# Performance work log

Hardware: AMD Instinct MI355X
Metric: run time of the kernel (lower is better)

Reference implementation:

```python
import jax, jax.numpy as jnp
import numpy as np

E = 64      # routed experts
K = 2       # top-k
CAP = 1024


def setup_inputs() -> dict:
    key = jax.random.key(0)
    ks = jax.random.split(key, 5)
    S, B, D, DFF = 2048, 4, 1024, 1408
    x = jax.random.normal(ks[0], (S, B, D), jnp.float32)
    Wg = jax.random.normal(ks[1], (D, E), jnp.float32) * 0.02
    W1 = jax.random.normal(ks[2], (E, D, DFF), jnp.float32) * 0.02
    W3 = jax.random.normal(ks[3], (E, D, DFF), jnp.float32) * 0.02
    W2 = jax.random.normal(ks[4], (E, DFF, D), jnp.float32) * 0.02
    return {"x": x, "Wg": Wg, "W1": W1, "W3": W3, "W2": W2}


def _moe(x, Wg, W1, W3, W2):
    S, B, D = x.shape
    tokens = jnp.transpose(x, (1, 0, 2)).reshape(-1, D)       # [T, D], T = B*S
    T = tokens.shape[0]

    # --- gate: softmax -> top-k, renormalize, aux loss (GShard-style) ---
    logits = tokens @ Wg                                       # [T, E]
    probs = jax.nn.softmax(logits, axis=-1)
    topk_w, topk_idx = jax.lax.top_k(probs, K)                 # [T, K]
    topk_w = topk_w / jnp.sum(topk_w, axis=-1, keepdims=True)
    me = jnp.mean(probs, axis=0)                               # [E] mean prob
    ce = jnp.mean(jax.nn.one_hot(topk_idx, E, dtype=jnp.float32).sum(1), axis=0) / K
    l_aux = E * jnp.sum(me * ce)

    # --- dispatch: per-pair slot within its expert via cumsum of one-hots ---
    flat_e = topk_idx.reshape(-1)                              # [T*K]
    oh = jax.nn.one_hot(flat_e, E, dtype=jnp.int32)            # [T*K, E]
    pos = jnp.cumsum(oh, axis=0) - 1                           # slot per expert
    slot = jnp.take_along_axis(pos, flat_e[:, None], axis=1)[:, 0]  # [T*K]
    keep = slot < CAP
    slot = jnp.where(keep, slot, 0)
    xr = jnp.repeat(tokens, K, axis=0)                         # [T*K, D]
    xr = jnp.where(keep[:, None], xr, 0.0)
    buf = jnp.zeros((E, CAP, D), x.dtype).at[flat_e, slot].add(xr)  # [E, C, D]

    # --- grouped expert FFN: SiLU-gated MLP per expert ---
    h = jax.nn.silu(jnp.einsum('ecd,edf->ecf', buf, W1)) * jnp.einsum('ecd,edf->ecf', buf, W3)
    eo = jnp.einsum('ecf,efd->ecd', h, W2)                     # [E, C, D]

    # --- combine: gather back, weight by gate probs, sum over k ---
    gathered = eo[flat_e, slot] * keep[:, None].astype(x.dtype)  # [T*K, D]
    combined = jnp.sum(gathered.reshape(T, K, D) * topk_w[..., None], axis=1)
    y = jnp.transpose(combined.reshape(B, S, D), (1, 0, 2))    # back to [S, B, D]
    return y, l_aux


def reference(x, Wg, W1, W3, W2):
    return _moe(x, Wg, W1, W3, W2)
```

## Files before the change

### kernel.cpp

```cpp
#include <hip/hip_runtime.h>
#include <hip/hip_bf16.h>


#define S_ 2048
#define B_ 4
#define D_ 1024
#define DFF_ 1408
#define E_ 64
#define T_ 8192
#define KTOP_ 2
#define NPAIR_ (T_*KTOP_)
#define PAD_ 384
#define ROWS_ (E_*PAD_)

#define BM 128
#define BN 128
#define BK 32

typedef __attribute__((ext_vector_type(8))) short short8;
typedef __attribute__((ext_vector_type(4))) short s16x4;
typedef __attribute__((ext_vector_type(4))) float f32x4;
typedef __attribute__((ext_vector_type(4))) unsigned short us4;

constexpr size_t OFF_PROBS  = 0;
constexpr size_t OFF_COUNTS = OFF_PROBS + (size_t)T_*E_*4;
constexpr size_t OFF_MESUM  = OFF_COUNTS + 512;
constexpr size_t OFF_ROWTOK = OFF_MESUM + 256;
constexpr size_t OFF_ROWW   = OFF_ROWTOK + (size_t)ROWS_*4;
constexpr size_t OFF_XBUF   = OFF_ROWW + (size_t)ROWS_*4;
constexpr size_t OFF_H      = OFF_XBUF + (size_t)ROWS_*D_*2;

__device__ __forceinline__ short f2bfs(float f) {
  union { __hip_bfloat16 h; short s; } u;
  u.h = __float2bfloat16(f);
  return u.s;
}

__device__ __forceinline__ int SWZ(int g) { return g ^ (((g >> 4) & 3) << 1); }

#define BARS() do {                                  \
    __builtin_amdgcn_sched_barrier(0);               \
    __builtin_amdgcn_s_barrier();                    \
    __builtin_amdgcn_sched_barrier(0);               \
  } while (0)
#define BARX() __builtin_amdgcn_s_barrier()
#define WAIT_LGKM0() asm volatile("s_waitcnt lgkmcnt(0)" ::: "memory")

__device__ __forceinline__ float softmax64(float acc, int lane) {
  float m = acc;
  for (int o = 32; o; o >>= 1) m = fmaxf(m, __shfl_xor(m, o));
  float p = expf(acc - m);
  float s = p;
  for (int o = 32; o; o >>= 1) s += __shfl_xor(s, o);
  return p / s;
}

__global__ __launch_bounds__(256) void gate_kernel(
    const float* __restrict__ x, const float* __restrict__ Wg,
    float* __restrict__ probs, int* __restrict__ counts,
    int* __restrict__ rowtok, float* __restrict__ roww,
    unsigned short* __restrict__ xbufO) {
  int t0 = blockIdx.x * 8;
  int tid = threadIdx.x;
  int lane = tid & 63, wv = tid >> 6;
  __shared__ float tk[8][D_];
  __shared__ int sE[8][2];
  __shared__ int sM[8][2];
  for (int u = tid; u < 8 * (D_ / 4); u += 256) {
    int r = u >> 8, c4 = u & 255;
    int t = t0 + r;
    int b = t >> 11, s = t & (S_ - 1);
    ((float4*)tk[r])[c4] = ((const float4*)(x + (size_t)(s * B_ + b) * D_))[c4];
  }
  __syncthreads();
  const float* tkA = tk[2 * wv];
  const float* tkB = tk[2 * wv + 1];
  float acc0 = 0.f, acc1 = 0.f;
  #pragma unroll 8
  for (int d = 0; d < D_; ++d) {
    float w = Wg[(size_t)d * E_ + lane];
    acc0 += tkA[d] * w;
    acc1 += tkB[d] * w;
  }
  #pragma unroll
  for (int half = 0; half < 2; ++half) {
    float p = softmax64(half ? acc1 : acc0, lane);
    int tkn = 2 * wv + half;
    int t = t0 + tkn;
    probs[(size_t)t * E_ + lane] = p;
    float v1 = p; int i1 = lane;
    for (int o = 32; o; o >>= 1) {
      float ov = __shfl_xor(v1, o); int oi = __shfl_xor(i1, o);
      if (ov > v1 || (ov == v1 && oi < i1)) { v1 = ov; i1 = oi; }
    }
    float v2 = (lane == i1) ? -1.f : p; int i2 = lane;
    for (int o = 32; o; o >>= 1) {
      float ov = __shfl_xor(v2, o); int oi = __shfl_xor(i2, o);
      if (ov > v2 || (ov == v2 && oi < i2)) { v2 = ov; i2 = oi; }
    }
    if (lane == 0) {
      float wsum = v1 + v2;
      int s1 = atomicAdd(&counts[i1], 1);
      int s2 = atomicAdd(&counts[i2], 1);
      int m1 = (s1 < PAD_) ? s1 : -1;
      int m2 = (s2 < PAD_) ? s2 : -1;
      if (m1 >= 0) { rowtok[i1 * PAD_ + m1] = t; roww[i1 * PAD_ + m1] = v1 / wsum; }
      if (m2 >= 0) { rowtok[i2 * PAD_ + m2] = t; roww[i2 * PAD_ + m2] = v2 / wsum; }
      sE[tkn][0] = i1; sM[tkn][0] = m1;
      sE[tkn][1] = i2; sM[tkn][1] = m2;
    }
  }
  __syncthreads();
  int hh = tid >> 7, t7 = tid & 127;
  #pragma unroll
  for (int pp = 0; pp < 8; ++pp) {
    int pr = 2 * pp + hh;
    int tkn = pr >> 1, j = pr & 1;
    int e = sE[tkn][j];
    int m = sM[tkn][j];
    if (m >= 0) {
      const float* src = tk[tkn] + t7 * 8;
      short8 g;
      #pragma unroll
      for (int k = 0; k < 8; ++k) g[k] = f2bfs(src[k]);
      *(short8*)(xbufO + (size_t)e * D_ * PAD_ + ((size_t)t7 * PAD_ + m) * 8) = g;
    }
  }
}

__global__ __launch_bounds__(256) void me_kernel(const float* __restrict__ probs,
                                                 float* __restrict__ mesum) {
  int e = blockIdx.x, tid = threadIdx.x;
  float a = 0.f;
  for (int t = tid; t < T_; t += 256) a += probs[(size_t)t * E_ + e];
  __shared__ float red[256];
  red[tid] = a; __syncthreads();
  for (int s = 128; s; s >>= 1) {
    if (tid < s) red[tid] += red[tid + s];
    __syncthreads();
  }
  if (tid == 0) mesum[e] = red[0];
}

__global__ __launch_bounds__(64) void finalize_kernel(
    const int* __restrict__ counts, const float* __restrict__ mesum,
    float* __restrict__ laux_out) {
  int lane = threadIdx.x;
  float contrib = (mesum[lane] / (float)T_) * ((float)counts[lane] / (float)(T_ * KTOP_));
  for (int o = 32; o; o >>= 1) contrib += __shfl_xor(contrib, o);
  if (lane == 0) laux_out[0] = (float)E_ * contrib;
}

__global__ __launch_bounds__(256, 2) void ffn1_kernel(
    const unsigned short* __restrict__ xbufO, const float* __restrict__ W1,
    const float* __restrict__ W3, const int* __restrict__ counts,
    unsigned short* __restrict__ hO) {
  int bid = blockIdx.x;
  int r = bid & 7, u = bid >> 3;
  int mb = u % 3; int v = u / 3;
  int ni = v % 11; int eg = v / 11;
  int e = eg * 8 + r;
  int n0 = ni * BN;
  int m0 = mb * BM;
  int Me = min(counts[e], PAD_);
  if (m0 >= Me) return;

  const unsigned short* AO = xbufO + (size_t)e * D_ * PAD_;
  const float* B1p = W1 + (size_t)e * D_ * DFF_ + n0;
  const float* B3p = W3 + (size_t)e * D_ * DFF_ + n0;
  unsigned short* hE = hO + (size_t)e * PAD_ * DFF_;

  __shared__ short B1s[2 * BK * BN];
  __shared__ short B3s[2 * BK * BN];
  __shared__ short Hb[BM * BN];

  int tid = threadIdx.x;
  int lane = tid & 63;
  int wv = tid >> 6, wr = wv >> 1, wc = wv & 1;

  int msel = tid >> 7;
  int t7 = tid & 127;
  int col4 = t7 & 31;
  int krow0 = (t7 >> 5) << 3;
  const float* qB = (msel ? B3p : B1p) + (size_t)krow0 * DFF_ + col4 * 4;
  char* Bdst = (char*)(msel ? B3s : B1s);
  int kseg = krow0 >> 3;
  int boffc[4];
  #pragma unroll
  for (int cc = 0; cc < 4; ++cc) {
    int c = col4 * 4 + cc;
    boffc[cc] = ((c >> 4) << 10) + (SWZ((kseg << 4) + (c & 15)) << 4);
  }

  const unsigned short* qa =
      AO + (((size_t)(lane >> 4)) * PAD_ + m0 + (wr << 6) + (lane & 15)) * 8;

  short8 afE[4], afO[4];
  f32x4 fBE[8], fBO[8];
  f32x4 acc1[4][4] = {};
  f32x4 acc3[4][4] = {};

#define F1_ALOAD(SET) do {                                               \
    _Pragma("unroll")                                                    \
    for (int mi = 0; mi < 4; ++mi)                                       \
      af##SET[mi] = *(const short8*)(qa + mi * 128);                     \
    qa += (size_t)4 * PAD_ * 8;                                          \
  } while (0)

#define F1_BLOAD(SET) do {                                               \
    _Pragma("unroll")                                                    \
    for (int j = 0; j < 8; ++j)                                          \
      fB##SET[j] = *(const f32x4*)(qB + (size_t)j * DFF_);               \
    qB += (size_t)BK * DFF_;                                             \
  } while (0)

#define F1_BWRITE(SET, BUF) do {                                         \
    _Pragma("unroll")                                                    \
    for (int cc = 0; cc < 4; ++cc) {                                     \
      short8 w;                                                          \
      _Pragma("unroll")                                                  \
      for (int j = 0; j < 8; ++j) w[j] = f2bfs(fB##SET[j][cc]);          \
      *(short8*)(Bdst + (BUF)*8192 + boffc[cc]) = w;                     \
    }                                                                    \
  } while (0)

#define F1_MFMA(BUF, SET) do {                                           \
    int lsw = SWZ(lane) << 4;                                            \
    __builtin_amdgcn_s_setprio(1);                                       \
    _Pragma("unroll")                                                    \
    for (int q = 0; q < 4; ++q) {                                        \
      short8 bf1 = *(const short8*)((char*)B1s + (BUF)*8192 + (((wc << 2) + q) << 10) + lsw); \
      short8 bf3 = *(const short8*)((char*)B3s + (BUF)*8192 + (((wc << 2) + q) << 10) + lsw); \
      _Pragma("unroll")                                                  \
      for (int mi = 0; mi < 4; ++mi) {                                   \
        acc1[mi][q] = __builtin_amdgcn_mfma_f32_16x16x32_bf16(af##SET[mi], bf1, acc1[mi][q], 0, 0, 0); \
        acc3[mi][q] = __builtin_amdgcn_mfma_f32_16x16x32_bf16(af##SET[mi], bf3, acc3[mi][q], 0, 0, 0); \
      }                                                                  \
    }                                                                    \
    __builtin_amdgcn_s_setprio(0);                                       \
  } while (0)

  F1_ALOAD(E); F1_BLOAD(E);
  F1_ALOAD(O); F1_BLOAD(O);
  for (int it = 0; it < 15; ++it) {
    F1_BWRITE(E, 0); WAIT_LGKM0(); BARS();
    F1_BLOAD(E);
    F1_MFMA(0, E);
    F1_ALOAD(E);
    BARX();
    F1_BWRITE(O, 1); WAIT_LGKM0(); BARS();
    F1_BLOAD(O);
    F1_MFMA(1, O);
    F1_ALOAD(O);
    BARX();
  }
  F1_BWRITE(E, 0); WAIT_LGKM0(); BARS(); F1_MFMA(0, E); BARX();
  F1_BWRITE(O, 1); WAIT_LGKM0(); BARS(); F1_MFMA(1, O);

  __syncthreads();
  int lr = (lane >> 4) << 2, lc = lane & 15;
  #pragma unroll
  for (int mi = 0; mi < 4; ++mi) {
    #pragma unroll
    for (int j = 0; j < 4; ++j) {
      int m = ((wr << 2) + mi) * 16 + lr + j;
      #pragma unroll
      for (int q = 0; q < 4; ++q) {
        int c = (wc << 6) + (q << 4) + lc;
        float a = acc1[mi][q][j];
        float gt = a / (1.f + __expf(-a));
        Hb[((size_t)(c >> 3) * BM + m) * 8 + (c & 7)] = f2bfs(gt * acc3[mi][q][j]);
      }
    }
  }
  __syncthreads();
  int co = tid >> 4, ml0 = (tid & 15) << 3;
  size_t fo = (size_t)(n0 >> 3) + co;
  #pragma unroll
  for (int i = 0; i < 8; ++i) {
    int ml = ml0 + i;
    short8 vq = *(const short8*)(Hb + ((size_t)co * BM + ml) * 8);
    *(short8*)(hE + (fo * PAD_ + m0 + ml) * 8) = vq;
  }
}

__global__ __launch_bounds__(256, 3) void ffn2_kernel(
    const unsigned short* __restrict__ hO, const float* __restrict__ W2,
    const int* __restrict__ counts, const int* __restrict__ rowtok,
    const float* __restrict__ roww, float* __restrict__ y) {
  int bid = blockIdx.x;
  int r = bid & 7, u = bid >> 3;
  int mb = u % 3; int v = u / 3;
  int ni = v % 8; int eg = v / 8;
  int e = eg * 8 + r;
  int n0 = ni * BN;
  int m0 = mb * BM;
  int Me = min(counts[e], PAD_);
  if (m0 >= Me) return;

  const unsigned short* AO = hO + (size_t)e * PAD_ * DFF_;
  const float* Bw = W2 + (size_t)e * DFF_ * D_ + n0;

  __shared__ short Bs[2 * BK * BN];

  int tid = threadIdx.x;
  int lane = tid & 63;
  int wv = tid >> 6, wr = wv >> 1, wc = wv & 1;

  int col4 = tid & 31;
  int krow0 = (tid >> 5) << 2;
  const float* qB = Bw + (size_t)krow0 * D_ + col4 * 4;
  int kseg = krow0 >> 3, khalf8 = ((krow0 >> 2) & 1) << 3;
  int boffc[4];
  #pragma unroll
  for (int cc = 0; cc < 4; ++cc) {
    int c = col4 * 4 + cc;
    boffc[cc] = ((c >> 4) << 10) + (SWZ((kseg << 4) + (c & 15)) << 4) + khalf8;
  }

  const unsigned short* qa =
      AO + (((size_t)(lane >> 4)) * PAD_ + m0 + (wr << 6) + (lane & 15)) * 8;

  short8 afE[4], afO[4];
  f32x4 fBE[4], fBO[4];
  f32x4 acc[4][4] = {};

#define F2_ALOAD(SET) do {                                               \
    _Pragma("unroll")                                                    \
    for (int mi = 0; mi < 4; ++mi)                                       \
      af##SET[mi] = *(const short8*)(qa + mi * 128);                     \
    qa += (size_t)4 * PAD_ * 8;                                          \
  } while (0)

#define F2_BLOAD(SET) do {                                               \
    _Pragma("unroll")                                                    \
    for (int j = 0; j < 4; ++j)                                          \
      fB##SET[j] = *(const f32x4*)(qB + (size_t)j * D_);                 \
    qB += (size_t)BK * D_;                                               \
  } while (0)

#define F2_BWRITE(SET, BUF) do {                                         \
    _Pragma("unroll")                                                    \
    for (int cc = 0; cc < 4; ++cc) {                                     \
      s16x4 w;                                                           \
      _Pragma("unroll")                                                  \
      for (int j = 0; j < 4; ++j) w[j] = f2bfs(fB##SET[j][cc]);          \
      *(s16x4*)((char*)Bs + (BUF)*8192 + boffc[cc]) = w;                 \
    }                                                                    \
  } while (0)

#define F2_MFMA(BUF, SET) do {                                           \
    int lsw = SWZ(lane) << 4;                                            \
    __builtin_amdgcn_s_setprio(1);                                       \
    _Pragma("unroll")                                                    \
    for (int q = 0; q < 4; ++q) {                                        \
      short8 bfr = *(const short8*)((char*)Bs + (BUF)*8192 + (((wc << 2) + q) << 10) + lsw); \
      _Pragma("unroll")                                                  \
      for (int mi = 0; mi < 4; ++mi)                                     \
        acc[mi][q] = __builtin_amdgcn_mfma_f32_16x16x32_bf16(af##SET[mi], bfr, acc[mi][q], 0, 0, 0); \
    }                                                                    \
    __builtin_amdgcn_s_setprio(0);                                       \
  } while (0)

  F2_ALOAD(E); F2_BLOAD(E);
  F2_ALOAD(O); F2_BLOAD(O);
  for (int it = 0; it < 21; ++it) {
    F2_BWRITE(E, 0); WAIT_LGKM0(); BARS();
    F2_BLOAD(E);
    F2_MFMA(0, E);
    F2_ALOAD(E);
    BARX();
    F2_BWRITE(O, 1); WAIT_LGKM0(); BARS();
    F2_BLOAD(O);
    F2_MFMA(1, O);
    F2_ALOAD(O);
    BARX();
  }
  F2_BWRITE(E, 0); WAIT_LGKM0(); BARS(); F2_MFMA(0, E); BARX();
  F2_BWRITE(O, 1); WAIT_LGKM0(); BARS(); F2_MFMA(1, O);

  int lr = (lane >> 4) << 2, lc = lane & 15;
  #pragma unroll
  for (int mi = 0; mi < 4; ++mi) {
    #pragma unroll
    for (int j = 0; j < 4; ++j) {
      int m = m0 + ((wr << 2) + mi) * 16 + lr + j;
      if (m < Me) {
        int rw = e * PAD_ + m;
        int t = rowtok[rw];
        float w = roww[rw];
        int b = t >> 11, s = t & (S_ - 1);
        float* yp = y + (size_t)(s * B_ + b) * D_ + n0 + (wc << 6) + lc;
        #pragma unroll
        for (int q = 0; q < 4; ++q)
          atomicAdd(&yp[q << 4], w * acc[mi][q][j]);
      }
    }
  }
}

extern "C" void kernel_launch(void* const* d_in, const int* in_sizes, int n_in,
                              void* d_out, int out_size, void* d_ws, size_t ws_size,
                              hipStream_t stream) {
  const float* x  = (const float*)d_in[0];
  const float* Wg = (const float*)d_in[1];
  const float* W1 = (const float*)d_in[2];
  const float* W3 = (const float*)d_in[3];
  const float* W2 = (const float*)d_in[4];
  float* y = (float*)d_out;
  float* laux = y + (size_t)S_ * B_ * D_;

  char* ws = (char*)d_ws;
  float* probs  = (float*)(ws + OFF_PROBS);
  int*   counts = (int*)  (ws + OFF_COUNTS);
  float* mesum  = (float*)(ws + OFF_MESUM);
  int*   rowtok = (int*)  (ws + OFF_ROWTOK);
  float* roww   = (float*)(ws + OFF_ROWW);
  unsigned short* xbufO = (unsigned short*)(ws + OFF_XBUF);
  unsigned short* hO    = (unsigned short*)(ws + OFF_H);

  hipMemsetAsync(d_out, 0, (size_t)out_size * sizeof(float), stream);
  hipMemsetAsync(counts, 0, 512, stream);

  gate_kernel<<<T_ / 8, 256, 0, stream>>>(x, Wg, probs, counts, rowtok, roww, xbufO);
  me_kernel<<<E_, 256, 0, stream>>>(probs, mesum);
  finalize_kernel<<<1, 64, 0, stream>>>(counts, mesum, laux);
  ffn1_kernel<<<8 * 8 * 11 * 3, 256, 0, stream>>>(xbufO, W1, W3, counts, hO);
  ffn2_kernel<<<8 * 8 * 8 * 3, 256, 0, stream>>>(hO, W2, counts, rowtok, roww, y);
}
```

Before: 579.9 us.

## Replace atomic scatter in FFN2 epilogue with bf16 store plus gather combine kernel

The FFN2 epilogue no longer atomically adds weighted fp32 results into the output. It now writes per-expert outputs as bf16 into the reused dispatch buffer. A new combine kernel reads each token's two expert rows using per-pair (expert, slot, weight) records from the gate, and writes y once with vector stores. This removes the output memset and the float atomics. The cost is an extra kernel launch, an extra round trip through the intermediate buffer, and bf16 rounding of expert outputs before the weighted sum.

```diff
diff --git a/kernel.cpp b/kernel.cpp
--- a/kernel.cpp
+++ b/kernel.cpp
@@ -25,15 +25,20 @@
 constexpr size_t OFF_PROBS  = 0;
 constexpr size_t OFF_COUNTS = OFF_PROBS + (size_t)T_*E_*4;
 constexpr size_t OFF_MESUM  = OFF_COUNTS + 512;
-constexpr size_t OFF_ROWTOK = OFF_MESUM + 256;
-constexpr size_t OFF_ROWW   = OFF_ROWTOK + (size_t)ROWS_*4;
-constexpr size_t OFF_XBUF   = OFF_ROWW + (size_t)ROWS_*4;
+constexpr size_t OFF_PAIRE  = OFF_MESUM + 256;
+constexpr size_t OFF_PAIRM  = OFF_PAIRE + (size_t)NPAIR_*4;
+constexpr size_t OFF_PAIRW  = OFF_PAIRM + (size_t)NPAIR_*4;
+constexpr size_t OFF_XBUF   = OFF_PAIRW + (size_t)NPAIR_*4;
 constexpr size_t OFF_H      = OFF_XBUF + (size_t)ROWS_*D_*2;
 
 __device__ __forceinline__ short f2bfs(float f) {
   union { __hip_bfloat16 h; short s; } u;
   u.h = __float2bfloat16(f);
   return u.s;
+}
+__device__ __forceinline__ float bf2f(unsigned short u) {
+  unsigned v = ((unsigned)u) << 16;
+  return __uint_as_float(v);
 }
 
 __device__ __forceinline__ int SWZ(int g) { return g ^ (((g >> 4) & 3) << 1); }
@@ -58,7 +63,7 @@
 __global__ __launch_bounds__(256) void gate_kernel(
     const float* __restrict__ x, const float* __restrict__ Wg,
     float* __restrict__ probs, int* __restrict__ counts,
-    int* __restrict__ rowtok, float* __restrict__ roww,
+    int* __restrict__ pairE, int* __restrict__ pairM, float* __restrict__ pairW,
     unsigned short* __restrict__ xbufO) {
   int t0 = blockIdx.x * 8;
   int tid = threadIdx.x;
@@ -104,8 +109,8 @@
       int s2 = atomicAdd(&counts[i2], 1);
       int m1 = (s1 < PAD_) ? s1 : -1;
       int m2 = (s2 < PAD_) ? s2 : -1;
-      if (m1 >= 0) { rowtok[i1 * PAD_ + m1] = t; roww[i1 * PAD_ + m1] = v1 / wsum; }
-      if (m2 >= 0) { rowtok[i2 * PAD_ + m2] = t; roww[i2 * PAD_ + m2] = v2 / wsum; }
+      pairE[2 * t]     = i1; pairM[2 * t]     = m1; pairW[2 * t]     = v1 / wsum;
+      pairE[2 * t + 1] = i2; pairM[2 * t + 1] = m2; pairW[2 * t + 1] = v2 / wsum;
       sE[tkn][0] = i1; sM[tkn][0] = m1;
       sE[tkn][1] = i2; sM[tkn][1] = m2;
     }
@@ -286,8 +291,7 @@
 
 __global__ __launch_bounds__(256, 3) void ffn2_kernel(
     const unsigned short* __restrict__ hO, const float* __restrict__ W2,
-    const int* __restrict__ counts, const int* __restrict__ rowtok,
-    const float* __restrict__ roww, float* __restrict__ y) {
+    const int* __restrict__ counts, unsigned short* __restrict__ eoO) {
   int bid = blockIdx.x;
   int r = bid & 7, u = bid >> 3;
   int mb = u % 3; int v = u / 3;
@@ -379,6 +383,7 @@
   F2_BWRITE(E, 0); WAIT_LGKM0(); BARS(); F2_MFMA(0, E); BARX();
   F2_BWRITE(O, 1); WAIT_LGKM0(); BARS(); F2_MFMA(1, O);
 
+  unsigned short* eoE = eoO + (size_t)e * PAD_ * D_;
   int lr = (lane >> 4) << 2, lc = lane & 15;
   #pragma unroll
   for (int mi = 0; mi < 4; ++mi) {
@@ -386,16 +391,51 @@
     for (int j = 0; j < 4; ++j) {
       int m = m0 + ((wr << 2) + mi) * 16 + lr + j;
       if (m < Me) {
-        int rw = e * PAD_ + m;
-        int t = rowtok[rw];
-        float w = roww[rw];
-        int b = t >> 11, s = t & (S_ - 1);
-        float* yp = y + (size_t)(s * B_ + b) * D_ + n0 + (wc << 6) + lc;
+        unsigned short* op = eoE + (size_t)m * D_ + n0 + (wc << 6) + lc;
         #pragma unroll
         for (int q = 0; q < 4; ++q)
-          atomicAdd(&yp[q << 4], w * acc[mi][q][j]);
+          op[q << 4] = (unsigned short)f2bfs(acc[mi][q][j]);
       }
     }
+  }
+}
+
+__global__ __launch_bounds__(256) void combine_kernel(
+    const unsigned short* __restrict__ eoO, const int* __restrict__ pairE,
+    const int* __restrict__ pairM, const float* __restrict__ pairW,
+    float* __restrict__ y) {
+  int t = blockIdx.x * 4 + (threadIdx.x >> 6);
+  int lane = threadIdx.x & 63;
+  int e1 = pairE[2 * t], m1 = pairM[2 * t];
+  int e2 = pairE[2 * t + 1], m2 = pairM[2 * t + 1];
+  float w1 = pairW[2 * t], w2 = pairW[2 * t + 1];
+  float out[16];
+  #pragma unroll
+  for (int i = 0; i < 16; ++i) out[i] = 0.f;
+  if (m1 >= 0) {
+    const unsigned short* rp = eoO + ((size_t)e1 * PAD_ + m1) * D_ + lane * 16;
+    short8 a = *(const short8*)rp, b = *(const short8*)(rp + 8);
+    #pragma unroll
+    for (int i = 0; i < 8; ++i) {
+      out[i]     += w1 * bf2f((unsigned short)a[i]);
+      out[8 + i] += w1 * bf2f((unsigned short)b[i]);
+    }
+  }
+  if (m2 >= 0) {
+    const unsigned short* rp = eoO + ((size_t)e2 * PAD_ + m2) * D_ + lane * 16;
+    short8 a = *(const short8*)rp, b = *(const short8*)(rp + 8);
+    #pragma unroll
+    for (int i = 0; i < 8; ++i) {
+      out[i]     += w2 * bf2f((unsigned short)a[i]);
+      out[8 + i] += w2 * bf2f((unsigned short)b[i]);
+    }
+  }
+  int b = t >> 11, s = t & (S_ - 1);
+  float* yp = y + (size_t)(s * B_ + b) * D_ + lane * 16;
+  #pragma unroll
+  for (int v = 0; v < 4; ++v) {
+    float4 o4 = make_float4(out[v * 4], out[v * 4 + 1], out[v * 4 + 2], out[v * 4 + 3]);
+    *(float4*)(yp + v * 4) = o4;
   }
 }
 
@@ -414,17 +454,18 @@
   float* probs  = (float*)(ws + OFF_PROBS);
   int*   counts = (int*)  (ws + OFF_COUNTS);
   float* mesum  = (float*)(ws + OFF_MESUM);
-  int*   rowtok = (int*)  (ws + OFF_ROWTOK);
-  float* roww   = (float*)(ws + OFF_ROWW);
+  int*   pairE  = (int*)  (ws + OFF_PAIRE);
+  int*   pairM  = (int*)  (ws + OFF_PAIRM);
+  float* pairW  = (float*)(ws + OFF_PAIRW);
   unsigned short* xbufO = (unsigned short*)(ws + OFF_XBUF);
   unsigned short* hO    = (unsigned short*)(ws + OFF_H);
 
-  hipMemsetAsync(d_out, 0, (size_t)out_size * sizeof(float), stream);
   hipMemsetAsync(counts, 0, 512, stream);
 
-  gate_kernel<<<T_ / 8, 256, 0, stream>>>(x, Wg, probs, counts, rowtok, roww, xbufO);
+  gate_kernel<<<T_ / 8, 256, 0, stream>>>(x, Wg, probs, counts, pairE, pairM, pairW, xbufO);
   me_kernel<<<E_, 256, 0, stream>>>(probs, mesum);
   finalize_kernel<<<1, 64, 0, stream>>>(counts, mesum, laux);
   ffn1_kernel<<<8 * 8 * 11 * 3, 256, 0, stream>>>(xbufO, W1, W3, counts, hO);
-  ffn2_kernel<<<8 * 8 * 8 * 3, 256, 0, stream>>>(hO, W2, counts, rowtok, roww, y);
-}
+  ffn2_kernel<<<8 * 8 * 8 * 3, 256, 0, stream>>>(hO, W2, counts, xbufO);
+  combine_kernel<<<T_ / 4, 256, 0, stream>>>(xbufO, pairE, pairM, pairW, y);
+}
```

Result: faster. 566.2 us (-2.4%).
